# Kernel optimization log

Measured on AMD Instinct MI355X. Metric: run time of the kernel, lower is better.

## Reference

```python
import jax, jax.numpy as jnp
import numpy as np

B, LQ, LKV = 2, 4096, 1024
QUERY_DIM, CROSS_DIM = 512, 768
HEADS, DIM_HEAD = 8, 64
INNER = HEADS * DIM_HEAD
SCALE = DIM_HEAD ** -0.5


def setup_inputs() -> dict:
    key = jax.random.key(0)
    ks = jax.random.split(key, 7)
    s = 0.02
    return {
        "hidden_states": jax.random.normal(ks[0], (B, LQ, QUERY_DIM), jnp.float32),
        "encoder_hidden_states": jax.random.normal(ks[1], (B, LKV, CROSS_DIM), jnp.float32),
        "Wq": jax.random.normal(ks[2], (QUERY_DIM, INNER), jnp.float32) * s,
        "Wk": jax.random.normal(ks[3], (CROSS_DIM, INNER), jnp.float32) * s,
        "Wv": jax.random.normal(ks[4], (CROSS_DIM, INNER), jnp.float32) * s,
        "Wo": jax.random.normal(ks[5], (INNER, QUERY_DIM), jnp.float32) * s,
        "bo": jnp.zeros((QUERY_DIM,), jnp.float32),
    }


def reference(hidden_states, encoder_hidden_states, Wq, Wk, Wv, Wo, bo):
    # Projections
    q = hidden_states @ Wq                 # [B, Lq, inner]
    k = encoder_hidden_states @ Wk         # [B, Lkv, inner]
    v = encoder_hidden_states @ Wv         # [B, Lkv, inner]
    # Split heads: [B, H, L, Dh]
    q = q.reshape(B, LQ, HEADS, DIM_HEAD).transpose(0, 2, 1, 3)
    k = k.reshape(B, LKV, HEADS, DIM_HEAD).transpose(0, 2, 1, 3)
    v = v.reshape(B, LKV, HEADS, DIM_HEAD).transpose(0, 2, 1, 3)
    # Scores [B, H, Lq, Lkv], softmax over Lkv
    scores = jnp.einsum("bhqd,bhkd->bhqk", q, k) * SCALE
    attn = jax.nn.softmax(scores, axis=-1)
    out = jnp.einsum("bhqk,bhkd->bhqd", attn, v)  # [B, H, Lq, Dh]
    out = out.transpose(0, 2, 1, 3).reshape(B, LQ, INNER)
    return out @ Wo + bo                   # [B, Lq, query_dim]
```

## Files before the change

### kernel.cpp

```cpp
#include <hip/hip_runtime.h>
#include <hip/hip_bf16.h>
#include <math.h>

#define BB 2
#define LQ 4096
#define LKV 1024
#define QDIM 512
#define CDIM 768
#define HEADS 8
#define DHEAD 64
#define INNER 512
#define SCALE 0.125f

#define C1 0.18033688011112042f
#define C2 5.7707801635558535f

typedef __bf16 bf16x4 __attribute__((ext_vector_type(4)));
typedef __bf16 bf16x8 __attribute__((ext_vector_type(8)));
typedef float f32x4 __attribute__((ext_vector_type(4)));

__global__ __launch_bounds__(256)
void prep_weights(const float* __restrict__ Wq, const float* __restrict__ Wk,
                  const float* __restrict__ Wv, const float* __restrict__ Wo,
                  __bf16* __restrict__ Wq_t, __bf16* __restrict__ Wkv_t,
                  __bf16* __restrict__ Wo_t) {
    __shared__ float tile[32][33];
    int id = blockIdx.x;
    const float* W; __bf16* Out; int K;
    if (id < 256)       { W = Wq; Out = Wq_t; K = 512; }
    else if (id < 640)  { id -= 256;  W = Wk; Out = Wkv_t; K = 768; }
    else if (id < 1024) { id -= 640;  W = Wv; Out = Wkv_t + (size_t)512 * 768; K = 768; }
    else                { id -= 1024; W = Wo; Out = Wo_t; K = 512; }
    const int NT = 512 / 32;
    int kt = id / NT, nt = id % NT;
    const int t = threadIdx.x;
    int r = t >> 3, c4 = (t & 7) * 4;
    float4 v = *(const float4*)&W[(size_t)(kt * 32 + r) * 512 + nt * 32 + c4];
    tile[r][c4 + 0] = v.x; tile[r][c4 + 1] = v.y; tile[r][c4 + 2] = v.z; tile[r][c4 + 3] = v.w;
    __syncthreads();
    bf16x4 o = { (__bf16)tile[c4 + 0][r], (__bf16)tile[c4 + 1][r],
                 (__bf16)tile[c4 + 2][r], (__bf16)tile[c4 + 3][r] };
    *(bf16x4*)&Out[(size_t)(nt * 32 + r) * K + kt * 32 + c4] = o;
}

template<int BM, int BN, bool AF32, bool F32OUT, bool VTEP>
__global__ __launch_bounds__(256)
void gemm_t(const void* __restrict__ Av, const __bf16* __restrict__ Bt,
            __bf16* __restrict__ Cb, float* __restrict__ Cf, const float* __restrict__ bias,
            __bf16* __restrict__ VT, int M, int N, int K, int CN) {
    constexpr int WM = BM / 2, WN = BN / 2, FM = WM / 16, FN = WN / 16;
    constexpr int AJ4 = BM / 32;
    constexpr int AJ8 = BM / 64;
    constexpr int BJ8 = BN / 64;
    __shared__ __align__(16) __bf16 As[2][BM * 32];
    __shared__ __align__(16) __bf16 Bs[2][BN * 32];
    const int t = threadIdx.x;
    const int lane = t & 63;
    const int w = t >> 6;
    const int wm = w >> 1, wn = w & 1;
    const int bm = blockIdx.x * BM, bn = blockIdx.y * BN;
    const float* Af = (const float*)Av;
    const __bf16* Ab = (const __bf16*)Av;
    f32x4 acc[FM][FN] = {};
    const int rr = lane & 15, kb8 = (lane >> 4) * 8;
    const int NK = K / 32;

    float4 rA[AJ4];
    bf16x8 rAb[AJ8];
    bf16x8 rB[BJ8];

    auto loadA = [&](int kt) {
        if (AF32) {
            #pragma unroll
            for (int j = 0; j < AJ4; j++) {
                int q = t + 256 * j;
                rA[j] = *(const float4*)&Af[(size_t)(bm + (q >> 3)) * K + kt * 32 + (q & 7) * 4];
            }
        } else {
            #pragma unroll
            for (int j = 0; j < AJ8; j++) {
                int c = t + 256 * j;
                rAb[j] = *(const bf16x8*)&Ab[(size_t)(bm + (c >> 2)) * K + kt * 32 + (c & 3) * 8];
            }
        }
    };
    auto loadB = [&](int kt) {
        #pragma unroll
        for (int j = 0; j < BJ8; j++) {
            int c = t + 256 * j;
            rB[j] = *(const bf16x8*)&Bt[(size_t)(bn + (c >> 2)) * K + kt * 32 + (c & 3) * 8];
        }
    };
    auto writeBuf = [&](int buf) {
        if (AF32) {
            #pragma unroll
            for (int j = 0; j < AJ4; j++) {
                int q = t + 256 * j;
                bf16x4 o = { (__bf16)rA[j].x, (__bf16)rA[j].y, (__bf16)rA[j].z, (__bf16)rA[j].w };
                *(bf16x4*)&As[buf][q * 4] = o;
            }
        } else {
            #pragma unroll
            for (int j = 0; j < AJ8; j++) {
                int c = t + 256 * j;
                *(bf16x8*)&As[buf][c * 8] = rAb[j];
            }
        }
        #pragma unroll
        for (int j = 0; j < BJ8; j++) {
            int c = t + 256 * j;
            *(bf16x8*)&Bs[buf][c * 8] = rB[j];
        }
    };

    loadA(0); loadB(0);
    writeBuf(0);
    loadA(1); loadB(1);
    __syncthreads();

    for (int kt = 0; kt < NK; kt++) {
        const int cur = kt & 1;
        if (kt > 0) __syncthreads();
        if (kt + 1 < NK) writeBuf(cur ^ 1);
        if (kt + 2 < NK) { loadA(kt + 2); loadB(kt + 2); }
        bf16x8 a[FM], b[FN];
        #pragma unroll
        for (int f = 0; f < FM; f++) a[f] = *(const bf16x8*)&As[cur][(wm * WM + f * 16 + rr) * 32 + kb8];
        #pragma unroll
        for (int f = 0; f < FN; f++) b[f] = *(const bf16x8*)&Bs[cur][(wn * WN + f * 16 + rr) * 32 + kb8];
        __builtin_amdgcn_s_setprio(1);
        #pragma unroll
        for (int fm = 0; fm < FM; fm++)
            #pragma unroll
            for (int fn = 0; fn < FN; fn++)
                acc[fm][fn] = __builtin_amdgcn_mfma_f32_16x16x32_bf16(a[fm], b[fn], acc[fm][fn], 0, 0, 0);
        __builtin_amdgcn_s_setprio(0);
    }

    const int colg = lane & 15;
    const int rowg = (lane >> 4) * 4;
    if (VTEP && bn >= 512) {
        __syncthreads();
        __bf16* T = &As[0][0];
        #pragma unroll
        for (int fm = 0; fm < FM; fm++)
            #pragma unroll
            for (int fn = 0; fn < FN; fn++) {
                int dcol = wn * WN + fn * 16 + colg;
                int kvr  = wm * WM + fm * 16 + rowg;
                bf16x4 pv = { (__bf16)acc[fm][fn][0], (__bf16)acc[fm][fn][1],
                              (__bf16)acc[fm][fn][2], (__bf16)acc[fm][fn][3] };
                *(bf16x4*)((char*)T + ((dcol * 128 + kvr * 2) ^ ((dcol & 7) << 4))) = pv;
            }
        __syncthreads();
        int d = t >> 2, ch = t & 3;
        int base = d * 128 + ch * 32;
        bf16x8 o0 = *(const bf16x8*)((const char*)T + ((base) ^ ((d & 7) << 4)));
        bf16x8 o1 = *(const bf16x8*)((const char*)T + ((base + 16) ^ ((d & 7) << 4)));
        int b = bm >> 10, kv0 = bm & 1023, h = (bn - 512) >> 6;
        size_t vrow = (size_t)((b * 8 + h) * 64 + d);
        *(bf16x8*)&VT[vrow * 1024 + kv0 + ch * 16] = o0;
        *(bf16x8*)&VT[vrow * 1024 + kv0 + ch * 16 + 8] = o1;
    } else {
        #pragma unroll
        for (int fm = 0; fm < FM; fm++)
            #pragma unroll
            for (int fn = 0; fn < FN; fn++)
                #pragma unroll
                for (int r = 0; r < 4; r++) {
                    int row = bm + wm * WM + fm * 16 + rowg + r;
                    int col = bn + wn * WN + fn * 16 + colg;
                    float v = acc[fm][fn][r];
                    if (F32OUT) Cf[(size_t)row * CN + col] = v + bias[col];
                    else        Cb[(size_t)row * CN + col] = (__bf16)v;
                }
    }
}

__global__ __launch_bounds__(512, 4)
void attn4(const __bf16* __restrict__ Q, const __bf16* __restrict__ Kb,
           const __bf16* __restrict__ VT, __bf16* __restrict__ O) {
    __shared__ __align__(16) __bf16 SQ[128 * 64];
    __shared__ __align__(16) __bf16 Ks[2][64 * 64];
    __shared__ __align__(16) __bf16 Vs[2][64 * 64];
    const int t = threadIdx.x;
    const int lane = t & 63;
    const int w = t >> 6;
    const int bh = blockIdx.y;
    const int b = bh >> 3, h = bh & 7;
    const int qbase = b * LQ + blockIdx.x * 128;
    const int kvbase = b * LKV;
    const int hq = h * 64;
    const int q16 = lane & 15;
    const int hh = lane >> 4;

    #pragma unroll
    for (int i = 0; i < 2; i++) {
        int c = t + 512 * i;
        int row = c >> 3;
        bf16x8 v = *(const bf16x8*)&Q[(size_t)(qbase + row) * INNER + hq + (c & 7) * 8];
        *(bf16x8*)((char*)SQ + ((row * 128 + (c & 7) * 16) ^ ((row & 7) << 4))) = v;
    }

    const int srow = t >> 3;
    const int soff = ((srow * 128 + (t & 7) * 16) ^ ((srow & 7) << 4));
    bf16x8 kr, vr;
    kr = *(const bf16x8*)&Kb[(size_t)(kvbase + srow) * 512 + hq + (t & 7) * 8];
    vr = *(const bf16x8*)&VT[((size_t)bh * 64 + srow) * 1024 + (t & 7) * 8];
    *(bf16x8*)((char*)Ks[0] + soff) = kr;
    *(bf16x8*)((char*)Vs[0] + soff) = vr;
    kr = *(const bf16x8*)&Kb[(size_t)(kvbase + 64 + srow) * 512 + hq + (t & 7) * 8];
    vr = *(const bf16x8*)&VT[((size_t)bh * 64 + srow) * 1024 + 64 + (t & 7) * 8];
    __syncthreads();

    const int qrow = w * 16 + q16;
    const int rsw = (q16 & 7) << 4;
    bf16x8 qf0 = *(const bf16x8*)((const char*)SQ + ((qrow * 128 + hh * 16) ^ rsw));
    bf16x8 qf1 = *(const bf16x8*)((const char*)SQ + ((qrow * 128 + 64 + hh * 16) ^ rsw));
    bf16x8 ones;
    #pragma unroll
    for (int j = 0; j < 8; j++) ones[j] = (__bf16)1.0f;

    f32x4 acc_o[4] = {};
    f32x4 acc_l = {};

    const int NT = LKV / 64;
    for (int kt = 0; kt < NT; kt++) {
        const int cur = kt & 1;
        if (kt > 0) __syncthreads();
        if (kt + 1 < NT) {
            const int nxt = cur ^ 1;
            *(bf16x8*)((char*)Ks[nxt] + soff) = kr;
            *(bf16x8*)((char*)Vs[nxt] + soff) = vr;
        }
        if (kt + 2 < NT) {
            kr = *(const bf16x8*)&Kb[(size_t)(kvbase + (kt + 2) * 64 + srow) * 512 + hq + (t & 7) * 8];
            vr = *(const bf16x8*)&VT[((size_t)bh * 64 + srow) * 1024 + (kt + 2) * 64 + (t & 7) * 8];
        }

        f32x4 s[4];
        __builtin_amdgcn_s_setprio(1);
        #pragma unroll
        for (int kvf = 0; kvf < 4; kvf++) {
            int krow = kvf * 16 + q16;
            bf16x8 k0 = *(const bf16x8*)((const char*)Ks[cur] + ((krow * 128 + hh * 16) ^ rsw));
            bf16x8 k1 = *(const bf16x8*)((const char*)Ks[cur] + ((krow * 128 + 64 + hh * 16) ^ rsw));
            f32x4 sa = {};
            sa = __builtin_amdgcn_mfma_f32_16x16x32_bf16(k0, qf0, sa, 0, 0, 0);
            sa = __builtin_amdgcn_mfma_f32_16x16x32_bf16(k1, qf1, sa, 0, 0, 0);
            s[kvf] = sa;
        }
        __builtin_amdgcn_s_setprio(0);

        #pragma unroll
        for (int kvf = 0; kvf < 4; kvf++) {
            bf16x4 pv;
            #pragma unroll
            for (int r = 0; r < 4; r++)
                pv[r] = (__bf16)exp2f(__builtin_fmaf(s[kvf][r], C1, -C2));
            *(bf16x4*)((char*)SQ + ((qrow * 128 + kvf * 32 + hh * 8) ^ rsw)) = pv;
        }
        bf16x8 pa0 = *(const bf16x8*)((const char*)SQ + ((qrow * 128 + hh * 16) ^ rsw));
        bf16x8 pa1 = *(const bf16x8*)((const char*)SQ + ((qrow * 128 + 64 + hh * 16) ^ rsw));

        __builtin_amdgcn_s_setprio(1);
        acc_l = __builtin_amdgcn_mfma_f32_16x16x32_bf16(pa0, ones, acc_l, 0, 0, 0);
        acc_l = __builtin_amdgcn_mfma_f32_16x16x32_bf16(pa1, ones, acc_l, 0, 0, 0);
        #pragma unroll
        for (int df = 0; df < 4; df++) {
            int vrow = df * 16 + q16;
            bf16x8 v0 = *(const bf16x8*)((const char*)Vs[cur] + ((vrow * 128 + hh * 16) ^ rsw));
            bf16x8 v1 = *(const bf16x8*)((const char*)Vs[cur] + ((vrow * 128 + 64 + hh * 16) ^ rsw));
            acc_o[df] = __builtin_amdgcn_mfma_f32_16x16x32_bf16(pa0, v0, acc_o[df], 0, 0, 0);
            acc_o[df] = __builtin_amdgcn_mfma_f32_16x16x32_bf16(pa1, v1, acc_o[df], 0, 0, 0);
        }
        __builtin_amdgcn_s_setprio(0);
    }

    #pragma unroll
    for (int df = 0; df < 4; df++)
        #pragma unroll
        for (int r = 0; r < 4; r++) {
            float v = acc_o[df][r] / acc_l[r];
            int row = w * 16 + hh * 4 + r;
            int col = df * 16 + q16;
            *(__bf16*)((char*)SQ + ((row * 128 + col * 2) ^ ((row & 7) << 4))) = (__bf16)v;
        }
    __syncthreads();
    #pragma unroll
    for (int i = 0; i < 2; i++) {
        int c = t + 512 * i;
        int row = c >> 3;
        bf16x8 v = *(const bf16x8*)((const char*)SQ + ((row * 128 + (c & 7) * 16) ^ ((row & 7) << 4)));
        *(bf16x8*)&O[(size_t)(qbase + row) * INNER + hq + (c & 7) * 8] = v;
    }
}

extern "C" void kernel_launch(void* const* d_in, const int* in_sizes, int n_in,
                              void* d_out, int out_size, void* d_ws, size_t ws_size,
                              hipStream_t stream) {
    const float* hs  = (const float*)d_in[0];
    const float* ehs = (const float*)d_in[1];
    const float* Wq  = (const float*)d_in[2];
    const float* Wk  = (const float*)d_in[3];
    const float* Wv  = (const float*)d_in[4];
    const float* Wo  = (const float*)d_in[5];
    const float* bo  = (const float*)d_in[6];
    float* out = (float*)d_out;

    char* ws = (char*)d_ws;
    size_t off = 0;
    auto alloc = [&](size_t nbytes) {
        char* p = ws + off;
        off += (nbytes + 255) & ~(size_t)255;
        return p;
    };
    __bf16* Wq_t  = (__bf16*)alloc((size_t)QDIM * INNER * 2);
    __bf16* Wkv_t = (__bf16*)alloc((size_t)CDIM * INNER * 2 * 2);
    __bf16* Wo_t  = (__bf16*)alloc((size_t)INNER * QDIM * 2);
    __bf16* Qb    = (__bf16*)alloc((size_t)BB * LQ * INNER * 2);
    __bf16* Kbb   = (__bf16*)alloc((size_t)BB * LKV * INNER * 2);
    __bf16* VTb   = (__bf16*)alloc((size_t)BB * HEADS * DHEAD * LKV * 2);
    __bf16* AOb   = (__bf16*)alloc((size_t)BB * LQ * INNER * 2);

    prep_weights<<<dim3(1280), dim3(256), 0, stream>>>(Wq, Wk, Wv, Wo, Wq_t, Wkv_t, Wo_t);

    gemm_t<64, 128, true, false, false><<<dim3(BB * LQ / 64, INNER / 128), dim3(256), 0, stream>>>(
        hs, Wq_t, Qb, nullptr, nullptr, nullptr, BB * LQ, INNER, QDIM, INNER);
    gemm_t<64, 64, true, false, true><<<dim3(BB * LKV / 64, 1024 / 64), dim3(256), 0, stream>>>(
        ehs, Wkv_t, Kbb, nullptr, nullptr, VTb, BB * LKV, 1024, CDIM, INNER);
    attn4<<<dim3(LQ / 128, BB * HEADS), dim3(512), 0, stream>>>(Qb, Kbb, VTb, AOb);
    gemm_t<64, 128, false, true, false><<<dim3(BB * LQ / 64, QDIM / 128), dim3(256), 0, stream>>>(
        AOb, Wo_t, nullptr, out, bo, nullptr, BB * LQ, QDIM, INNER, QDIM);
}
```

Before: 74.43 us.

## Give attention waves two query groups each and widen GEMM K tile

The attention kernel moves from 8 waves of 16 query rows to 4 waves of 32 rows. Each K/V fragment read from shared memory now feeds MFMAs for two query groups, which halves LDS traffic per FLOP. The projection GEMMs also gain a BK template parameter set to 64, halving the number of K-loop iterations and barriers. In exchange, register pressure rises and attention has fewer threads per block, which may reduce latency hiding.

Result: slower. 79.96 us (+7.4%).

```diff
diff --git a/kernel.cpp b/kernel.cpp
--- a/kernel.cpp
+++ b/kernel.cpp
@@ -43,17 +43,18 @@
     *(bf16x4*)&Out[(size_t)(nt * 32 + r) * K + kt * 32 + c4] = o;
 }
 
-template<int BM, int BN, bool AF32, bool F32OUT, bool VTEP>
+template<int BM, int BN, int BK, bool AF32, bool F32OUT, bool VTEP>
 __global__ __launch_bounds__(256)
 void gemm_t(const void* __restrict__ Av, const __bf16* __restrict__ Bt,
             __bf16* __restrict__ Cb, float* __restrict__ Cf, const float* __restrict__ bias,
             __bf16* __restrict__ VT, int M, int N, int K, int CN) {
     constexpr int WM = BM / 2, WN = BN / 2, FM = WM / 16, FN = WN / 16;
-    constexpr int AJ4 = BM / 32;
-    constexpr int AJ8 = BM / 64;
-    constexpr int BJ8 = BN / 64;
-    __shared__ __align__(16) __bf16 As[2][BM * 32];
-    __shared__ __align__(16) __bf16 Bs[2][BN * 32];
+    constexpr int KK = BK / 32;
+    constexpr int AQ4 = BM * BK / 1024;
+    constexpr int AC8 = BM * BK / 2048;
+    constexpr int BC8 = BN * BK / 2048;
+    __shared__ __align__(16) __bf16 As[2][BM * BK];
+    __shared__ __align__(16) __bf16 Bs[2][BN * BK];
     const int t = threadIdx.x;
     const int lane = t & 63;
     const int w = t >> 6;
@@ -63,51 +64,51 @@
     const __bf16* Ab = (const __bf16*)Av;
     f32x4 acc[FM][FN] = {};
     const int rr = lane & 15, kb8 = (lane >> 4) * 8;
-    const int NK = K / 32;
-
-    float4 rA[AJ4];
-    bf16x8 rAb[AJ8];
-    bf16x8 rB[BJ8];
+    const int NK = K / BK;
+
+    float4 rA[AQ4];
+    bf16x8 rAb[AC8];
+    bf16x8 rB[BC8];
 
     auto loadA = [&](int kt) {
         if (AF32) {
             #pragma unroll
-            for (int j = 0; j < AJ4; j++) {
+            for (int j = 0; j < AQ4; j++) {
                 int q = t + 256 * j;
-                rA[j] = *(const float4*)&Af[(size_t)(bm + (q >> 3)) * K + kt * 32 + (q & 7) * 4];
+                rA[j] = *(const float4*)&Af[(size_t)(bm + q / (BK / 4)) * K + kt * BK + (q % (BK / 4)) * 4];
             }
         } else {
             #pragma unroll
-            for (int j = 0; j < AJ8; j++) {
+            for (int j = 0; j < AC8; j++) {
                 int c = t + 256 * j;
-                rAb[j] = *(const bf16x8*)&Ab[(size_t)(bm + (c >> 2)) * K + kt * 32 + (c & 3) * 8];
+                rAb[j] = *(const bf16x8*)&Ab[(size_t)(bm + c / (BK / 8)) * K + kt * BK + (c % (BK / 8)) * 8];
             }
         }
     };
     auto loadB = [&](int kt) {
         #pragma unroll
-        for (int j = 0; j < BJ8; j++) {
+        for (int j = 0; j < BC8; j++) {
             int c = t + 256 * j;
-            rB[j] = *(const bf16x8*)&Bt[(size_t)(bn + (c >> 2)) * K + kt * 32 + (c & 3) * 8];
+            rB[j] = *(const bf16x8*)&Bt[(size_t)(bn + c / (BK / 8)) * K + kt * BK + (c % (BK / 8)) * 8];
         }
     };
     auto writeBuf = [&](int buf) {
         if (AF32) {
             #pragma unroll
-            for (int j = 0; j < AJ4; j++) {
+            for (int j = 0; j < AQ4; j++) {
                 int q = t + 256 * j;
                 bf16x4 o = { (__bf16)rA[j].x, (__bf16)rA[j].y, (__bf16)rA[j].z, (__bf16)rA[j].w };
                 *(bf16x4*)&As[buf][q * 4] = o;
             }
         } else {
             #pragma unroll
-            for (int j = 0; j < AJ8; j++) {
+            for (int j = 0; j < AC8; j++) {
                 int c = t + 256 * j;
                 *(bf16x8*)&As[buf][c * 8] = rAb[j];
             }
         }
         #pragma unroll
-        for (int j = 0; j < BJ8; j++) {
+        for (int j = 0; j < BC8; j++) {
             int c = t + 256 * j;
             *(bf16x8*)&Bs[buf][c * 8] = rB[j];
         }
@@ -115,7 +116,7 @@
 
     loadA(0); loadB(0);
     writeBuf(0);
-    loadA(1); loadB(1);
+    if (NK > 1) { loadA(1); loadB(1); }
     __syncthreads();
 
     for (int kt = 0; kt < NK; kt++) {
@@ -123,18 +124,21 @@
         if (kt > 0) __syncthreads();
         if (kt + 1 < NK) writeBuf(cur ^ 1);
         if (kt + 2 < NK) { loadA(kt + 2); loadB(kt + 2); }
-        bf16x8 a[FM], b[FN];
-        #pragma unroll
-        for (int f = 0; f < FM; f++) a[f] = *(const bf16x8*)&As[cur][(wm * WM + f * 16 + rr) * 32 + kb8];
-        #pragma unroll
-        for (int f = 0; f < FN; f++) b[f] = *(const bf16x8*)&Bs[cur][(wn * WN + f * 16 + rr) * 32 + kb8];
-        __builtin_amdgcn_s_setprio(1);
-        #pragma unroll
-        for (int fm = 0; fm < FM; fm++)
-            #pragma unroll
-            for (int fn = 0; fn < FN; fn++)
-                acc[fm][fn] = __builtin_amdgcn_mfma_f32_16x16x32_bf16(a[fm], b[fn], acc[fm][fn], 0, 0, 0);
-        __builtin_amdgcn_s_setprio(0);
+        #pragma unroll
+        for (int kk = 0; kk < KK; kk++) {
+            bf16x8 a[FM], b[FN];
+            #pragma unroll
+            for (int f = 0; f < FM; f++) a[f] = *(const bf16x8*)&As[cur][(wm * WM + f * 16 + rr) * BK + kk * 32 + kb8];
+            #pragma unroll
+            for (int f = 0; f < FN; f++) b[f] = *(const bf16x8*)&Bs[cur][(wn * WN + f * 16 + rr) * BK + kk * 32 + kb8];
+            __builtin_amdgcn_s_setprio(1);
+            #pragma unroll
+            for (int fm = 0; fm < FM; fm++)
+                #pragma unroll
+                for (int fn = 0; fn < FN; fn++)
+                    acc[fm][fn] = __builtin_amdgcn_mfma_f32_16x16x32_bf16(a[fm], b[fn], acc[fm][fn], 0, 0, 0);
+            __builtin_amdgcn_s_setprio(0);
+        }
     }
 
     const int colg = lane & 15;
@@ -177,8 +181,8 @@
     }
 }
 
-__global__ __launch_bounds__(512, 4)
-void attn4(const __bf16* __restrict__ Q, const __bf16* __restrict__ Kb,
+__global__ __launch_bounds__(256, 3)
+void attn5(const __bf16* __restrict__ Q, const __bf16* __restrict__ Kb,
            const __bf16* __restrict__ VT, __bf16* __restrict__ O) {
     __shared__ __align__(16) __bf16 SQ[128 * 64];
     __shared__ __align__(16) __bf16 Ks[2][64 * 64];
@@ -195,34 +199,51 @@
     const int hh = lane >> 4;
 
     #pragma unroll
-    for (int i = 0; i < 2; i++) {
-        int c = t + 512 * i;
+    for (int i = 0; i < 4; i++) {
+        int c = t + 256 * i;
         int row = c >> 3;
         bf16x8 v = *(const bf16x8*)&Q[(size_t)(qbase + row) * INNER + hq + (c & 7) * 8];
         *(bf16x8*)((char*)SQ + ((row * 128 + (c & 7) * 16) ^ ((row & 7) << 4))) = v;
     }
 
-    const int srow = t >> 3;
-    const int soff = ((srow * 128 + (t & 7) * 16) ^ ((srow & 7) << 4));
-    bf16x8 kr, vr;
-    kr = *(const bf16x8*)&Kb[(size_t)(kvbase + srow) * 512 + hq + (t & 7) * 8];
-    vr = *(const bf16x8*)&VT[((size_t)bh * 64 + srow) * 1024 + (t & 7) * 8];
-    *(bf16x8*)((char*)Ks[0] + soff) = kr;
-    *(bf16x8*)((char*)Vs[0] + soff) = vr;
-    kr = *(const bf16x8*)&Kb[(size_t)(kvbase + 64 + srow) * 512 + hq + (t & 7) * 8];
-    vr = *(const bf16x8*)&VT[((size_t)bh * 64 + srow) * 1024 + 64 + (t & 7) * 8];
+    int soff[2];
+    bf16x8 kr[2], vr[2];
+    #pragma unroll
+    for (int i = 0; i < 2; i++) {
+        int c = t + 256 * i;
+        int row = c >> 3, coff = (c & 7) * 8;
+        soff[i] = (row * 128 + (c & 7) * 16) ^ ((row & 7) << 4);
+        kr[i] = *(const bf16x8*)&Kb[(size_t)(kvbase + row) * 512 + hq + coff];
+        vr[i] = *(const bf16x8*)&VT[((size_t)bh * 64 + row) * 1024 + coff];
+    }
+    #pragma unroll
+    for (int i = 0; i < 2; i++) {
+        *(bf16x8*)((char*)Ks[0] + soff[i]) = kr[i];
+        *(bf16x8*)((char*)Vs[0] + soff[i]) = vr[i];
+    }
+    #pragma unroll
+    for (int i = 0; i < 2; i++) {
+        int c = t + 256 * i;
+        int row = c >> 3, coff = (c & 7) * 8;
+        kr[i] = *(const bf16x8*)&Kb[(size_t)(kvbase + 64 + row) * 512 + hq + coff];
+        vr[i] = *(const bf16x8*)&VT[((size_t)bh * 64 + row) * 1024 + 64 + coff];
+    }
     __syncthreads();
 
-    const int qrow = w * 16 + q16;
     const int rsw = (q16 & 7) << 4;
-    bf16x8 qf0 = *(const bf16x8*)((const char*)SQ + ((qrow * 128 + hh * 16) ^ rsw));
-    bf16x8 qf1 = *(const bf16x8*)((const char*)SQ + ((qrow * 128 + 64 + hh * 16) ^ rsw));
+    bf16x8 qf[2][2];
+    #pragma unroll
+    for (int g = 0; g < 2; g++) {
+        int qrow = w * 32 + g * 16 + q16;
+        qf[g][0] = *(const bf16x8*)((const char*)SQ + ((qrow * 128 + hh * 16) ^ rsw));
+        qf[g][1] = *(const bf16x8*)((const char*)SQ + ((qrow * 128 + 64 + hh * 16) ^ rsw));
+    }
     bf16x8 ones;
     #pragma unroll
     for (int j = 0; j < 8; j++) ones[j] = (__bf16)1.0f;
 
-    f32x4 acc_o[4] = {};
-    f32x4 acc_l = {};
+    f32x4 acc_o[2][4] = {};
+    f32x4 acc_l[2] = {};
 
     const int NT = LKV / 64;
     for (int kt = 0; kt < NT; kt++) {
@@ -230,66 +251,90 @@
         if (kt > 0) __syncthreads();
         if (kt + 1 < NT) {
             const int nxt = cur ^ 1;
-            *(bf16x8*)((char*)Ks[nxt] + soff) = kr;
-            *(bf16x8*)((char*)Vs[nxt] + soff) = vr;
+            #pragma unroll
+            for (int i = 0; i < 2; i++) {
+                *(bf16x8*)((char*)Ks[nxt] + soff[i]) = kr[i];
+                *(bf16x8*)((char*)Vs[nxt] + soff[i]) = vr[i];
+            }
         }
         if (kt + 2 < NT) {
-            kr = *(const bf16x8*)&Kb[(size_t)(kvbase + (kt + 2) * 64 + srow) * 512 + hq + (t & 7) * 8];
-            vr = *(const bf16x8*)&VT[((size_t)bh * 64 + srow) * 1024 + (kt + 2) * 64 + (t & 7) * 8];
-        }
-
-        f32x4 s[4];
+            #pragma unroll
+            for (int i = 0; i < 2; i++) {
+                int c = t + 256 * i;
+                int row = c >> 3, coff = (c & 7) * 8;
+                kr[i] = *(const bf16x8*)&Kb[(size_t)(kvbase + (kt + 2) * 64 + row) * 512 + hq + coff];
+                vr[i] = *(const bf16x8*)&VT[((size_t)bh * 64 + row) * 1024 + (kt + 2) * 64 + coff];
+            }
+        }
+
+        f32x4 s[2][4];
         __builtin_amdgcn_s_setprio(1);
         #pragma unroll
         for (int kvf = 0; kvf < 4; kvf++) {
             int krow = kvf * 16 + q16;
             bf16x8 k0 = *(const bf16x8*)((const char*)Ks[cur] + ((krow * 128 + hh * 16) ^ rsw));
             bf16x8 k1 = *(const bf16x8*)((const char*)Ks[cur] + ((krow * 128 + 64 + hh * 16) ^ rsw));
-            f32x4 sa = {};
-            sa = __builtin_amdgcn_mfma_f32_16x16x32_bf16(k0, qf0, sa, 0, 0, 0);
-            sa = __builtin_amdgcn_mfma_f32_16x16x32_bf16(k1, qf1, sa, 0, 0, 0);
-            s[kvf] = sa;
+            #pragma unroll
+            for (int g = 0; g < 2; g++) {
+                f32x4 sa = {};
+                sa = __builtin_amdgcn_mfma_f32_16x16x32_bf16(k0, qf[g][0], sa, 0, 0, 0);
+                sa = __builtin_amdgcn_mfma_f32_16x16x32_bf16(k1, qf[g][1], sa, 0, 0, 0);
+                s[g][kvf] = sa;
+            }
         }
         __builtin_amdgcn_s_setprio(0);
 
-        #pragma unroll
-        for (int kvf = 0; kvf < 4; kvf++) {
-            bf16x4 pv;
-            #pragma unroll
-            for (int r = 0; r < 4; r++)
-                pv[r] = (__bf16)exp2f(__builtin_fmaf(s[kvf][r], C1, -C2));
-            *(bf16x4*)((char*)SQ + ((qrow * 128 + kvf * 32 + hh * 8) ^ rsw)) = pv;
-        }
-        bf16x8 pa0 = *(const bf16x8*)((const char*)SQ + ((qrow * 128 + hh * 16) ^ rsw));
-        bf16x8 pa1 = *(const bf16x8*)((const char*)SQ + ((qrow * 128 + 64 + hh * 16) ^ rsw));
+        bf16x8 pa[2][2];
+        #pragma unroll
+        for (int g = 0; g < 2; g++) {
+            int qrow = w * 32 + g * 16 + q16;
+            #pragma unroll
+            for (int kvf = 0; kvf < 4; kvf++) {
+                bf16x4 pv;
+                #pragma unroll
+                for (int r = 0; r < 4; r++)
+                    pv[r] = (__bf16)exp2f(__builtin_fmaf(s[g][kvf][r], C1, -C2));
+                *(bf16x4*)((char*)SQ + ((qrow * 128 + kvf * 32 + hh * 8) ^ rsw)) = pv;
+            }
+            pa[g][0] = *(const bf16x8*)((const char*)SQ + ((qrow * 128 + hh * 16) ^ rsw));
+            pa[g][1] = *(const bf16x8*)((const char*)SQ + ((qrow * 128 + 64 + hh * 16) ^ rsw));
+        }
 
         __builtin_amdgcn_s_setprio(1);
-        acc_l = __builtin_amdgcn_mfma_f32_16x16x32_bf16(pa0, ones, acc_l, 0, 0, 0);
-        acc_l = __builtin_amdgcn_mfma_f32_16x16x32_bf16(pa1, ones, acc_l, 0, 0, 0);
+        #pragma unroll
+        for (int g = 0; g < 2; g++) {
+            acc_l[g] = __builtin_amdgcn_mfma_f32_16x16x32_bf16(pa[g][0], ones, acc_l[g], 0, 0, 0);
+            acc_l[g] = __builtin_amdgcn_mfma_f32_16x16x32_bf16(pa[g][1], ones, acc_l[g], 0, 0, 0);
+        }
         #pragma unroll
         for (int df = 0; df < 4; df++) {
             int vrow = df * 16 + q16;
             bf16x8 v0 = *(const bf16x8*)((const char*)Vs[cur] + ((vrow * 128 + hh * 16) ^ rsw));
             bf16x8 v1 = *(const bf16x8*)((const char*)Vs[cur] + ((vrow * 128 + 64 + hh * 16) ^ rsw));
-            acc_o[df] = __builtin_amdgcn_mfma_f32_16x16x32_bf16(pa0, v0, acc_o[df], 0, 0, 0);
-            acc_o[df] = __builtin_amdgcn_mfma_f32_16x16x32_bf16(pa1, v1, acc_o[df], 0, 0, 0);
+            #pragma unroll
+            for (int g = 0; g < 2; g++) {
+                acc_o[g][df] = __builtin_amdgcn_mfma_f32_16x16x32_bf16(pa[g][0], v0, acc_o[g][df], 0, 0, 0);
+                acc_o[g][df] = __builtin_amdgcn_mfma_f32_16x16x32_bf16(pa[g][1], v1, acc_o[g][df], 0, 0, 0);
+            }
         }
         __builtin_amdgcn_s_setprio(0);
     }
 
     #pragma unroll
-    for (int df = 0; df < 4; df++)
-        #pragma unroll
-        for (int r = 0; r < 4; r++) {
-            float v = acc_o[df][r] / acc_l[r];
-            int row = w * 16 + hh * 4 + r;
-            int col = df * 16 + q16;
-            *(__bf16*)((char*)SQ + ((row * 128 + col * 2) ^ ((row & 7) << 4))) = (__bf16)v;
-        }
+    for (int g = 0; g < 2; g++)
+        #pragma unroll
+        for (int df = 0; df < 4; df++)
+            #pragma unroll
+            for (int r = 0; r < 4; r++) {
+                float v = acc_o[g][df][r] / acc_l[g][r];
+                int row = w * 32 + g * 16 + hh * 4 + r;
+                int col = df * 16 + q16;
+                *(__bf16*)((char*)SQ + ((row * 128 + col * 2) ^ ((row & 7) << 4))) = (__bf16)v;
+            }
     __syncthreads();
     #pragma unroll
-    for (int i = 0; i < 2; i++) {
-        int c = t + 512 * i;
+    for (int i = 0; i < 4; i++) {
+        int c = t + 256 * i;
         int row = c >> 3;
         bf16x8 v = *(const bf16x8*)((const char*)SQ + ((row * 128 + (c & 7) * 16) ^ ((row & 7) << 4)));
         *(bf16x8*)&O[(size_t)(qbase + row) * INNER + hq + (c & 7) * 8] = v;
@@ -325,11 +370,11 @@
 
     prep_weights<<<dim3(1280), dim3(256), 0, stream>>>(Wq, Wk, Wv, Wo, Wq_t, Wkv_t, Wo_t);
 
-    gemm_t<64, 128, true, false, false><<<dim3(BB * LQ / 64, INNER / 128), dim3(256), 0, stream>>>(
+    gemm_t<64, 128, 64, true, false, false><<<dim3(BB * LQ / 64, INNER / 128), dim3(256), 0, stream>>>(
         hs, Wq_t, Qb, nullptr, nullptr, nullptr, BB * LQ, INNER, QDIM, INNER);
-    gemm_t<64, 64, true, false, true><<<dim3(BB * LKV / 64, 1024 / 64), dim3(256), 0, stream>>>(
+    gemm_t<64, 64, 64, true, false, true><<<dim3(BB * LKV / 64, 1024 / 64), dim3(256), 0, stream>>>(
         ehs, Wkv_t, Kbb, nullptr, nullptr, VTb, BB * LKV, 1024, CDIM, INNER);
-    attn4<<<dim3(LQ / 128, BB * HEADS), dim3(512), 0, stream>>>(Qb, Kbb, VTb, AOb);
-    gemm_t<64, 128, false, true, false><<<dim3(BB * LQ / 64, QDIM / 128), dim3(256), 0, stream>>>(
+    attn5<<<dim3(LQ / 128, BB * HEADS), dim3(256), 0, stream>>>(Qb, Kbb, VTb, AOb);
+    gemm_t<64, 128, 64, false, true, false><<<dim3(BB * LQ / 64, QDIM / 128), dim3(256), 0, stream>>>(
         AOb, Wo_t, nullptr, out, bo, nullptr, BB * LQ, QDIM, INNER, QDIM);
 }
```
